# Kernel optimization log

Hardware: AMD Instinct MI355X
Metric: run time of the kernel (lower is better)

Reference implementation:

```python
import jax, jax.numpy as jnp
import numpy as np

# -------- configuration (production-scale segmentation head) --------
BS, C, H, W = 8, 256, 96, 96
N = H * W          # nodes in the spanning tree (flattened pixels)
E = N - 1          # spanning-tree edge count
ZETA_G = 0.01      # default zeta_g of Global_APro.forward


def setup_inputs() -> dict:
    key = jax.random.key(0)
    k1, k2 = jax.random.split(key)
    feature_in = jax.random.normal(k1, (BS, 1, H, W), dtype=jnp.float32)
    # scaled so norm2 distances over C=256 channels stay O(1..10)
    embed_in = 0.1 * jax.random.normal(k2, (BS, C, H, W), dtype=jnp.float32)
    # Random spanning trees, one per batch element. Edges are topologically
    # ordered: edge e connects parent=src[e] < child=tgt[e]=e+1, so processing
    # edges in order is a valid root->leaf sweep (and reversed is leaf->root).
    rng = np.random.default_rng(0)
    trees = []
    children = np.arange(1, N, dtype=np.int32)
    for _ in range(BS):
        parents = np.floor(rng.random(E) * np.arange(1, N)).astype(np.int32)
        trees.append(np.stack([parents, children], axis=1))
    tree = jnp.asarray(np.stack(trees, axis=0))  # [BS, E, 2] int32
    return {"feature_in": feature_in, "embed_in": embed_in, "tree": tree}


def _gp_single(f, wgt, src, tgt):
    """Global affinity propagation (tree filter) on one tree.
    Computes out_i = sum_j A_ij f_j / sum_j A_ij with A_ij = prod of edge
    affinities along the unique tree path i->j, via the classic two-pass DP.
    f: [N], wgt/src/tgt: [E] (edges topologically ordered, parent=src).
    """
    ones = jnp.ones_like(f)

    def up(carry, xs):                 # leaf -> root aggregation
        S, Z = carry
        s, t, we = xs
        S = S.at[s].add(we * S[t])
        Z = Z.at[s].add(we * Z[t])
        return (S, Z), None

    (S, Z), _ = jax.lax.scan(up, (f, ones), (src, tgt, wgt), reverse=True)

    def down(carry, xs):               # root -> leaf propagation
        F, G = carry
        s, t, we = xs
        F = F.at[t].set(we * F[s] + (1.0 - we * we) * F[t])
        G = G.at[t].set(we * G[s] + (1.0 - we * we) * G[t])
        return (F, G), None

    (F, G), _ = jax.lax.scan(down, (S, Z), (src, tgt, wgt))
    return F / G


def reference(feature_in, embed_in, tree):
    bs, c, h, w = embed_in.shape
    n = h * w
    emb = embed_in.reshape(bs, c, n)               # [bs, c, N]
    src = tree[:, :, 0]                            # [bs, E]
    tgt = tree[:, :, 1]                            # [bs, E]
    # gather node embeddings along tree edges (get_true_index)
    gather = jax.vmap(lambda e, i: e[:, i])        # [c, N], [E] -> [c, E]
    src_node = gather(emb, src)                    # [bs, c, E]
    tgt_node = gather(emb, tgt)                    # [bs, c, E]
    diff = src_node - tgt_node
    dist = jnp.sum(diff * diff, axis=1)            # norm2_distance -> [bs, E]
    wgt = jnp.exp(-ZETA_G * dist)                  # edge affinity
    f = feature_in.reshape(bs, n)                  # [bs, N]
    out = jax.vmap(_gp_single)(f, wgt, src, tgt)   # [bs, N]
    return out.reshape(bs, 1, h, w)
```

## Files before the change

### kernel.cpp

```cpp
#include <hip/hip_runtime.h>
#include <hip/hip_bf16.h>
#include <hip/hip_fp16.h>

#define BS 8
#define C  256
#define N  9216
#define E  9215
#define MAXD 128
#define LVL_STRIDE 192
#define TSLABS (N / 64)

__global__ __launch_bounds__(1024) void setup_kernel(const float* __restrict__ emb,
                                                     __half* __restrict__ embT,
                                                     const int* __restrict__ tree,
                                                     int* __restrict__ uparr,
                                                     unsigned char* __restrict__ lenG,
                                                     int* __restrict__ lvlOff) {
    __shared__ int P[N];
    __shared__ unsigned int CC[N];
    __shared__ int cnt[MAXD];
    __shared__ int off[MAXD + 1];
    const int tid = threadIdx.x;

    if (blockIdx.x < BS) {
        const int b = blockIdx.x;
        const int* tb = tree + b * E * 2;

        for (int t = tid; t < N; t += 1024) {
            P[t] = (t == 0) ? 0 : (tb[(t - 1) * 2] | (1 << 16));
            CC[t] = 0u;
        }
        for (int i = tid; i < MAXD; i += 1024) cnt[i] = 0;
        __syncthreads();

        for (int it = 0; it < 6; ++it) {
            int np[9];
            int k = 0;
            for (int t = tid; t < N; t += 1024, ++k) {
                int p = P[t];
                int pa = P[p & 0xffff];
                np[k] = (pa & 0xffff) | ((p >> 16) + (pa >> 16)) << 16;
            }
            __syncthreads();
            k = 0;
            for (int t = tid; t < N; t += 1024, ++k) P[t] = np[k];
            __syncthreads();
        }

        for (int t = 1 + tid; t < N; t += 1024) {
            int d = P[t] >> 16; if (d > MAXD - 1) d = MAXD - 1;
            atomicAdd(&cnt[d], 1);
            int p = tb[(t - 1) * 2];
            atomicAdd(&CC[p], 1u);
        }
        __syncthreads();
        if (tid == 0) {
            int acc = 0, mx = 1;
            for (int d = 0; d < MAXD; ++d) {
                off[d] = acc; acc += cnt[d];
                if (cnt[d] > 0) mx = d;
            }
            off[MAXD] = acc;
            lvlOff[b * LVL_STRIDE + MAXD + 1] = mx;
        }
        __syncthreads();
        for (int i = tid; i < MAXD; i += 1024) cnt[i] = 0;
        __syncthreads();

        for (int p = tid; p < N; p += 1024) {
            unsigned int c = CC[p];
            if (c > 0) {
                int dlev = (P[p] >> 16) + 1; if (dlev > MAXD - 1) dlev = MAXD - 1;
                int base = off[dlev] + atomicAdd(&cnt[dlev], (int)c);
                P[p] = (P[p] & 0xffff0000) | base;
            }
        }
        for (int i = tid; i < N; i += 1024) lenG[b * N + i] = 0;
        __syncthreads();

        for (int p = tid; p < N; p += 1024) {
            unsigned int c = CC[p];
            if (c > 0) {
                int base = P[p] & 0xffff;
                unsigned char fl = (c > 2u) ? 4 : 0;
                for (unsigned int j = 0; j < c; j += 2) {
                    unsigned char ln = (j + 2 <= c) ? 2 : 1;
                    lenG[b * N + base + j] = ln | fl;
                }
            }
        }
        __syncthreads();

        for (int t = 1 + tid; t < N; t += 1024) {
            int p = tb[(t - 1) * 2];
            unsigned int o = atomicSub(&CC[p], 1u) - 1u;
            int slot = (P[p] & 0xffff) + (int)o;
            uparr[b * N + slot] = t | (p << 16);
        }
        for (int i = tid; i <= MAXD; i += 1024) lvlOff[b * LVL_STRIDE + i] = off[i];
    } else {
        const int tb = blockIdx.x - BS;
        const int b  = tb & 7;
        const int n0 = (tb >> 3) * 64;
        __half (*tile)[65] = (__half(*)[65])P;

        const int nn = tid & 63;
        const int cg = tid >> 6;
        const float* src = emb + (size_t)b * C * N + n0;
        #pragma unroll
        for (int k = 0; k < 16; ++k) {
            int cc = cg * 16 + k;
            tile[cc][nn] = __float2half(src[(size_t)cc * N + nn]);
        }
        __syncthreads();

        const int cp = tid & 127;
        const int ng = tid >> 7;
        __half* dst = embT + ((size_t)b * N + n0) * C;
        #pragma unroll
        for (int k = 0; k < 8; ++k) {
            int n2 = ng * 8 + k;
            __half2 v = __halves2half2(tile[2 * cp][n2], tile[2 * cp + 1][n2]);
            *(__half2*)(dst + (size_t)n2 * C + 2 * cp) = v;
        }
    }
}

__global__ __launch_bounds__(256) void weights_kernel(const __half* __restrict__ embT,
                                                      const int* __restrict__ tree,
                                                      float* __restrict__ wgt) {
    const int b   = blockIdx.y;
    const int tid = threadIdx.x;
    const int lane = tid & 63;
    const int wid  = tid >> 6;
    const int sub  = lane >> 5;
    const int l    = lane & 31;
    const int e    = (blockIdx.x * 4 + wid) * 2 + sub;

    float acc = 0.f;
    if (e < E) {
        int s = tree[(b * E + e) * 2];
        int t = tree[(b * E + e) * 2 + 1];
        const float4* ps = (const float4*)(embT + ((size_t)b * N + s) * C) + l;
        const float4* pt = (const float4*)(embT + ((size_t)b * N + t) * C) + l;
        float4 av = *ps;
        float4 bv = *pt;
        const __half2* ah = (const __half2*)&av;
        const __half2* bh = (const __half2*)&bv;
        #pragma unroll
        for (int j = 0; j < 4; ++j) {
            float2 fa = __half22float2(ah[j]);
            float2 fb = __half22float2(bh[j]);
            float d0 = fa.x - fb.x;
            float d1 = fa.y - fb.y;
            acc += d0 * d0 + d1 * d1;
        }
    }
    #pragma unroll
    for (int m = 16; m >= 1; m >>= 1) acc += __shfl_xor(acc, m);
    if (l == 0 && e < E) wgt[b * N + e] = __expf(-0.01f * acc);
}

__global__ __launch_bounds__(1024) void dp_kernel(const float* __restrict__ feat,
                                                  const int* __restrict__ lvlOff,
                                                  const int* __restrict__ uparr,
                                                  const unsigned char* __restrict__ lenG,
                                                  const float* __restrict__ wgt,
                                                  float* __restrict__ out) {
    const int b = blockIdx.x;
    const int tid = threadIdx.x;
    __shared__ float2 V[N];
    __shared__ int2 TSW[N];
    __shared__ unsigned char LEN[N];
    __shared__ int off[MAXD + 1];
    __shared__ int maxd_s;

    for (int i = tid; i <= MAXD; i += 1024) off[i] = lvlOff[b * LVL_STRIDE + i];
    if (tid == 0) maxd_s = lvlOff[b * LVL_STRIDE + MAXD + 1];

    const int* tsA = uparr + b * N;
    const float* wG = wgt + b * N;
    const unsigned char* lG = lenG + b * N;
    for (int i = tid; i < N; i += 1024) {
        V[i] = make_float2(feat[b * N + i], 1.0f);
        LEN[i] = lG[i];
    }
    for (int i = tid; i < E; i += 1024) {
        int ts = tsA[i];
        float w = wG[(ts & 0xffff) - 1];
        TSW[i] = make_int2(ts, __float_as_int(w));
    }
    __syncthreads();
    const int maxd = maxd_s;

    int s1 = off[maxd + 1];
    for (int lev = maxd; lev >= 1; --lev) {
        int s0 = off[lev];
        for (int i = s0 + tid; i < s1; i += 1024) {
            int lb = LEN[i];
            if (lb) {
                int2 e0 = TSW[i];
                int p = e0.x >> 16;
                float w0 = __int_as_float(e0.y);
                float2 v0 = V[e0.x & 0xffff];
                float ax = w0 * v0.x, ay = w0 * v0.y;
                if (lb & 2) {
                    int2 e1 = TSW[i + 1];
                    float w1 = __int_as_float(e1.y);
                    float2 v1 = V[e1.x & 0xffff];
                    ax += w1 * v1.x; ay += w1 * v1.y;
                }
                if (lb & 4) {
                    atomicAdd(&V[p].x, ax);
                    atomicAdd(&V[p].y, ay);
                } else {
                    float2 vp = V[p];
                    V[p] = make_float2(vp.x + ax, vp.y + ay);
                }
            }
        }
        s1 = s0;
        __syncthreads();
    }
    int s0 = off[1];
    for (int lev = 1; lev <= maxd; ++lev) {
        int s1d = off[lev + 1];
        for (int i = s0 + tid; i < s1d; i += 1024) {
            int2 ew = TSW[i];
            int t = ew.x & 0xffff, s = ew.x >> 16;
            float w = __int_as_float(ew.y);
            float2 vs = V[s], vt = V[t];
            float c = 1.f - w * w;
            V[t] = make_float2(w * vs.x + c * vt.x, w * vs.y + c * vt.y);
        }
        s0 = s1d;
        __syncthreads();
    }
    for (int i = tid; i < N; i += 1024) {
        float2 v = V[i];
        out[b * N + i] = v.x / v.y;
    }
}

extern "C" void kernel_launch(void* const* d_in, const int* in_sizes, int n_in,
                              void* d_out, int out_size, void* d_ws, size_t ws_size,
                              hipStream_t stream) {
    const float* feat = (const float*)d_in[0];
    const float* emb  = (const float*)d_in[1];
    const int*   tree = (const int*)d_in[2];
    float* out = (float*)d_out;

    const size_t BN = (size_t)BS * N;
    float* wgt    = (float*)d_ws;
    int*   uparr  = (int*)((char*)d_ws + BN * 4);
    int*   lvlOff = (int*)((char*)d_ws + BN * 8);
    unsigned char* lenG = (unsigned char*)((char*)d_ws + BN * 8 + BS * LVL_STRIDE * 4);
    __half* embT  = (__half*)((char*)d_ws +
                     ((BN * 9 + BS * LVL_STRIDE * 4 + 255) / 256) * 256);

    setup_kernel<<<BS + TSLABS * BS, 1024, 0, stream>>>(emb, embT, tree, uparr, lenG, lvlOff);
    weights_kernel<<<dim3((E + 7) / 8, BS), 256, 0, stream>>>(embT, tree, wgt);
    dp_kernel<<<BS, 1024, 0, stream>>>(feat, lvlOff, uparr, lenG, wgt, out);
}
```

Baseline: 171.4 us.

## Overlap tree-level setup with edge-weight computation and prefetch DP level data

The transpose now runs as its own kernel. Tree depth and level bucketing move into a kernel that also computes the edge weights, so the serial per-tree setup blocks overlap with the weight blocks. Setup replaces the tid==0 serial offset scan with per-subgroup counters and a parallel prefix scan, and uses ping-pong pointer jumping without a register staging array. The DP kernel loads LEN as ints and prefetches the next level's edge records into registers before processing the current level, hiding LDS latency between barriers. Costs are more register pressure and more complex indexing.

```diff
diff --git a/kernel.cpp b/kernel.cpp
--- a/kernel.cpp
+++ b/kernel.cpp
@@ -10,156 +10,203 @@
 #define LVL_STRIDE 192
 #define TSLABS (N / 64)
 
-__global__ __launch_bounds__(1024) void setup_kernel(const float* __restrict__ emb,
-                                                     __half* __restrict__ embT,
-                                                     const int* __restrict__ tree,
-                                                     int* __restrict__ uparr,
-                                                     unsigned char* __restrict__ lenG,
-                                                     int* __restrict__ lvlOff) {
+__global__ __launch_bounds__(1024) void transpose_kernel(const float* __restrict__ emb,
+                                                         __half* __restrict__ embT) {
+    const int tb = blockIdx.x;
+    const int b  = tb & 7;
+    const int n0 = (tb >> 3) * 64;
+    __shared__ __half tile[256][65];
+    const int tid = threadIdx.x;
+
+    const int nn = tid & 63;
+    const int cg = tid >> 6;
+    const float* src = emb + (size_t)b * C * N + n0;
+    #pragma unroll
+    for (int k = 0; k < 16; ++k) {
+        int cc = cg * 16 + k;
+        tile[cc][nn] = __float2half(src[(size_t)cc * N + nn]);
+    }
+    __syncthreads();
+
+    const int cp = tid & 127;
+    const int ng = tid >> 7;
+    __half* dst = embT + ((size_t)b * N + n0) * C;
+    #pragma unroll
+    for (int k = 0; k < 8; ++k) {
+        int n2 = ng * 8 + k;
+        __half2 v = __halves2half2(tile[2 * cp][n2], tile[2 * cp + 1][n2]);
+        *(__half2*)(dst + (size_t)n2 * C + 2 * cp) = v;
+    }
+}
+
+__global__ __launch_bounds__(1024) void wl_kernel(const __half* __restrict__ embT,
+                                                  const int* __restrict__ tree,
+                                                  float* __restrict__ wgt,
+                                                  int* __restrict__ uparr,
+                                                  unsigned char* __restrict__ lenG,
+                                                  int* __restrict__ lvlOff) {
     __shared__ int P[N];
-    __shared__ unsigned int CC[N];
-    __shared__ int cnt[MAXD];
+    __shared__ int Q[N];
+    __shared__ int cnt8[MAXD * 8];
+    __shared__ int tot[MAXD];
+    __shared__ int sc1[MAXD];
     __shared__ int off[MAXD + 1];
+    __shared__ int maxd_sh;
     const int tid = threadIdx.x;
 
-    if (blockIdx.x < BS) {
-        const int b = blockIdx.x;
-        const int* tb = tree + b * E * 2;
-
+    if (blockIdx.x >= BS) {
+        const int wb = blockIdx.x - BS;
+        const int b  = wb & 7;
+        const int l  = tid & 31;
+        const int e  = (wb >> 3) * 32 + (tid >> 5);
+        if (e < E) {
+            int s = tree[(b * E + e) * 2];
+            int t = tree[(b * E + e) * 2 + 1];
+            const float4* ps = (const float4*)(embT + ((size_t)b * N + s) * C) + l;
+            const float4* pt = (const float4*)(embT + ((size_t)b * N + t) * C) + l;
+            float4 av = *ps;
+            float4 bv = *pt;
+            const __half2* ah = (const __half2*)&av;
+            const __half2* bh = (const __half2*)&bv;
+            float acc = 0.f;
+            #pragma unroll
+            for (int j = 0; j < 4; ++j) {
+                float2 fa = __half22float2(ah[j]);
+                float2 fb = __half22float2(bh[j]);
+                float d0 = fa.x - fb.x;
+                float d1 = fa.y - fb.y;
+                acc += d0 * d0 + d1 * d1;
+            }
+            #pragma unroll
+            for (int m = 16; m >= 1; m >>= 1) acc += __shfl_xor(acc, m);
+            if (l == 0) wgt[b * N + e] = __expf(-0.01f * acc);
+        }
+        return;
+    }
+
+    const int b = blockIdx.x;
+    const int* tb = tree + b * E * 2;
+
+    for (int t = tid; t < N; t += 1024)
+        P[t] = (t == 0) ? 0 : (tb[(t - 1) * 2] | (1 << 16));
+    for (int i = tid; i < MAXD * 8; i += 1024) cnt8[i] = 0;
+    {
+        int* lz = (int*)(lenG + b * N);
+        for (int i = tid; i < N / 4; i += 1024) lz[i] = 0;
+    }
+    if (tid == 0) maxd_sh = 1;
+    __syncthreads();
+
+    for (int r = 0; r < 3; ++r) {
         for (int t = tid; t < N; t += 1024) {
-            P[t] = (t == 0) ? 0 : (tb[(t - 1) * 2] | (1 << 16));
-            CC[t] = 0u;
-        }
-        for (int i = tid; i < MAXD; i += 1024) cnt[i] = 0;
+            int p = P[t];
+            int pa = P[p & 0xffff];
+            Q[t] = (pa & 0xffff) | (((p >> 16) + (pa >> 16)) << 16);
+        }
         __syncthreads();
-
-        for (int it = 0; it < 6; ++it) {
-            int np[9];
-            int k = 0;
-            for (int t = tid; t < N; t += 1024, ++k) {
-                int p = P[t];
-                int pa = P[p & 0xffff];
-                np[k] = (pa & 0xffff) | ((p >> 16) + (pa >> 16)) << 16;
-            }
-            __syncthreads();
-            k = 0;
-            for (int t = tid; t < N; t += 1024, ++k) P[t] = np[k];
-            __syncthreads();
-        }
-
-        for (int t = 1 + tid; t < N; t += 1024) {
-            int d = P[t] >> 16; if (d > MAXD - 1) d = MAXD - 1;
-            atomicAdd(&cnt[d], 1);
-            int p = tb[(t - 1) * 2];
-            atomicAdd(&CC[p], 1u);
+        for (int t = tid; t < N; t += 1024) {
+            int p = Q[t];
+            int pa = Q[p & 0xffff];
+            P[t] = (pa & 0xffff) | (((p >> 16) + (pa >> 16)) << 16);
         }
         __syncthreads();
-        if (tid == 0) {
-            int acc = 0, mx = 1;
-            for (int d = 0; d < MAXD; ++d) {
-                off[d] = acc; acc += cnt[d];
-                if (cnt[d] > 0) mx = d;
-            }
-            off[MAXD] = acc;
-            lvlOff[b * LVL_STRIDE + MAXD + 1] = mx;
-        }
-        __syncthreads();
-        for (int i = tid; i < MAXD; i += 1024) cnt[i] = 0;
-        __syncthreads();
-
-        for (int p = tid; p < N; p += 1024) {
-            unsigned int c = CC[p];
-            if (c > 0) {
-                int dlev = (P[p] >> 16) + 1; if (dlev > MAXD - 1) dlev = MAXD - 1;
-                int base = off[dlev] + atomicAdd(&cnt[dlev], (int)c);
-                P[p] = (P[p] & 0xffff0000) | base;
-            }
-        }
-        for (int i = tid; i < N; i += 1024) lenG[b * N + i] = 0;
-        __syncthreads();
-
-        for (int p = tid; p < N; p += 1024) {
-            unsigned int c = CC[p];
-            if (c > 0) {
-                int base = P[p] & 0xffff;
-                unsigned char fl = (c > 2u) ? 4 : 0;
-                for (unsigned int j = 0; j < c; j += 2) {
-                    unsigned char ln = (j + 2 <= c) ? 2 : 1;
-                    lenG[b * N + base + j] = ln | fl;
-                }
-            }
-        }
-        __syncthreads();
-
-        for (int t = 1 + tid; t < N; t += 1024) {
-            int p = tb[(t - 1) * 2];
-            unsigned int o = atomicSub(&CC[p], 1u) - 1u;
-            int slot = (P[p] & 0xffff) + (int)o;
-            uparr[b * N + slot] = t | (p << 16);
-        }
-        for (int i = tid; i <= MAXD; i += 1024) lvlOff[b * LVL_STRIDE + i] = off[i];
-    } else {
-        const int tb = blockIdx.x - BS;
-        const int b  = tb & 7;
-        const int n0 = (tb >> 3) * 64;
-        __half (*tile)[65] = (__half(*)[65])P;
-
-        const int nn = tid & 63;
-        const int cg = tid >> 6;
-        const float* src = emb + (size_t)b * C * N + n0;
-        #pragma unroll
-        for (int k = 0; k < 16; ++k) {
-            int cc = cg * 16 + k;
-            tile[cc][nn] = __float2half(src[(size_t)cc * N + nn]);
-        }
-        __syncthreads();
-
-        const int cp = tid & 127;
-        const int ng = tid >> 7;
-        __half* dst = embT + ((size_t)b * N + n0) * C;
+    }
+
+    for (int t = tid; t < N; t += 1024) Q[t] = 0;
+    __syncthreads();
+    for (int t = 1 + tid; t < N; t += 1024) atomicAdd(&Q[tb[(t - 1) * 2]], 1);
+    __syncthreads();
+
+    for (int p = tid; p < N; p += 1024) {
+        int c = Q[p];
+        int dep = P[p] >> 16;
+        if (c > 0) {
+            int dlev = dep + 1;
+            int sub = tid >> 7;
+            int lo = atomicAdd(&cnt8[dlev * 8 + sub], c);
+            P[p] = (dep << 25) | (sub << 22) | lo;
+        } else {
+            P[p] = (dep << 25);
+        }
+    }
+    __syncthreads();
+
+    for (int d = tid; d < MAXD; d += 1024) {
+        int s = 0;
         #pragma unroll
         for (int k = 0; k < 8; ++k) {
-            int n2 = ng * 8 + k;
-            __half2 v = __halves2half2(tile[2 * cp][n2], tile[2 * cp + 1][n2]);
-            *(__half2*)(dst + (size_t)n2 * C + 2 * cp) = v;
-        }
-    }
+            int v = cnt8[d * 8 + k];
+            cnt8[d * 8 + k] = s;
+            s += v;
+        }
+        tot[d] = s;
+        if (s > 0) atomicMax(&maxd_sh, d);
+    }
+    __syncthreads();
+
+    {
+        int* src = tot; int* dst = sc1;
+        for (int step = 1; step < MAXD; step <<= 1) {
+            for (int d = tid; d < MAXD; d += 1024)
+                dst[d] = src[d] + ((d >= step) ? src[d - step] : 0);
+            __syncthreads();
+            int* tmp = src; src = dst; dst = tmp;
+        }
+        for (int d = tid; d < MAXD; d += 1024) off[d + 1] = src[d];
+        if (tid == 0) off[0] = 0;
+    }
+    __syncthreads();
+
+    for (int p = tid; p < N; p += 1024) {
+        int c = Q[p];
+        if (c > 0) {
+            int v = P[p];
+            int dep = ((unsigned)v) >> 25;
+            int sub = (v >> 22) & 7;
+            int lo  = v & 0x3FFF;
+            int dlev = dep + 1;
+            int base = off[dlev] + cnt8[dlev * 8 + sub] + lo;
+            P[p] = (dep << 25) | base;
+            unsigned char fl = (c > 2) ? 4 : 0;
+            for (int j = 0; j < c; j += 2)
+                lenG[b * N + base + j] = (unsigned char)(((j + 2 <= c) ? 2 : 1) | fl);
+        }
+    }
+    __syncthreads();
+
+    for (int t = 1 + tid; t < N; t += 1024) {
+        int p = tb[(t - 1) * 2];
+        unsigned int o = atomicSub((unsigned int*)&Q[p], 1u) - 1u;
+        int slot = (P[p] & 0x3FFF) + (int)o;
+        uparr[b * N + slot] = t | (p << 16);
+    }
+    for (int i = tid; i <= MAXD; i += 1024) lvlOff[b * LVL_STRIDE + i] = off[i];
+    if (tid == 0) lvlOff[b * LVL_STRIDE + MAXD + 1] = maxd_sh;
 }
 
-__global__ __launch_bounds__(256) void weights_kernel(const __half* __restrict__ embT,
-                                                      const int* __restrict__ tree,
-                                                      float* __restrict__ wgt) {
-    const int b   = blockIdx.y;
-    const int tid = threadIdx.x;
-    const int lane = tid & 63;
-    const int wid  = tid >> 6;
-    const int sub  = lane >> 5;
-    const int l    = lane & 31;
-    const int e    = (blockIdx.x * 4 + wid) * 2 + sub;
-
-    float acc = 0.f;
-    if (e < E) {
-        int s = tree[(b * E + e) * 2];
-        int t = tree[(b * E + e) * 2 + 1];
-        const float4* ps = (const float4*)(embT + ((size_t)b * N + s) * C) + l;
-        const float4* pt = (const float4*)(embT + ((size_t)b * N + t) * C) + l;
-        float4 av = *ps;
-        float4 bv = *pt;
-        const __half2* ah = (const __half2*)&av;
-        const __half2* bh = (const __half2*)&bv;
-        #pragma unroll
-        for (int j = 0; j < 4; ++j) {
-            float2 fa = __half22float2(ah[j]);
-            float2 fb = __half22float2(bh[j]);
-            float d0 = fa.x - fb.x;
-            float d1 = fa.y - fb.y;
-            acc += d0 * d0 + d1 * d1;
-        }
-    }
-    #pragma unroll
-    for (int m = 16; m >= 1; m >>= 1) acc += __shfl_xor(acc, m);
-    if (l == 0 && e < E) wgt[b * N + e] = __expf(-0.01f * acc);
-}
+#define UP_PROCESS(e0, e1, lb)                                                \
+    if (lb) {                                                                 \
+        int p_ = (e0).x >> 16;                                                \
+        float w0_ = __int_as_float((e0).y);                                   \
+        float2 v0_ = V[(e0).x & 0xffff];                                      \
+        float ax_ = w0_ * v0_.x, ay_ = w0_ * v0_.y;                           \
+        if ((lb) & 2) {                                                       \
+            float w1_ = __int_as_float((e1).y);                               \
+            float2 v1_ = V[(e1).x & 0xffff];                                  \
+            ax_ += w1_ * v1_.x; ay_ += w1_ * v1_.y;                           \
+        }                                                                     \
+        if ((lb) & 4) { atomicAdd(&V[p_].x, ax_); atomicAdd(&V[p_].y, ay_); } \
+        else { float2 vp_ = V[p_]; V[p_] = make_float2(vp_.x + ax_, vp_.y + ay_); } \
+    }
+
+#define DOWN_PROCESS(g)                                                       \
+    {                                                                         \
+        int t_ = (g).x & 0xffff, s_ = (g).x >> 16;                            \
+        float w_ = __int_as_float((g).y);                                     \
+        float2 vs_ = V[s_], vt_ = V[t_];                                      \
+        float c_ = 1.f - w_ * w_;                                             \
+        V[t_] = make_float2(w_ * vs_.x + c_ * vt_.x, w_ * vs_.y + c_ * vt_.y); \
+    }
 
 __global__ __launch_bounds__(1024) void dp_kernel(const float* __restrict__ feat,
                                                   const int* __restrict__ lvlOff,
@@ -171,7 +218,7 @@
     const int tid = threadIdx.x;
     __shared__ float2 V[N];
     __shared__ int2 TSW[N];
-    __shared__ unsigned char LEN[N];
+    __shared__ __align__(16) unsigned char LEN[N];
     __shared__ int off[MAXD + 1];
     __shared__ int maxd_s;
 
@@ -180,11 +227,11 @@
 
     const int* tsA = uparr + b * N;
     const float* wG = wgt + b * N;
-    const unsigned char* lG = lenG + b * N;
-    for (int i = tid; i < N; i += 1024) {
+    const int* lG4 = (const int*)(lenG + b * N);
+    for (int i = tid; i < N; i += 1024)
         V[i] = make_float2(feat[b * N + i], 1.0f);
-        LEN[i] = lG[i];
-    }
+    for (int i = tid; i < N / 4; i += 1024)
+        ((int*)LEN)[i] = lG4[i];
     for (int i = tid; i < E; i += 1024) {
         int ts = tsA[i];
         float w = wG[(ts & 0xffff) - 1];
@@ -194,48 +241,70 @@
     const int maxd = maxd_s;
 
     int s1 = off[maxd + 1];
+    int s0 = off[maxd];
+    int pns0 = (maxd >= 2) ? off[maxd - 1] : 0;
+    int2 eA0, eA1, eB0, eB1; int lbA, lbB;
+    {
+        int i0 = s0 + tid, i1 = i0 + 1024;
+        int c0 = (i0 < s1) ? i0 : 0;
+        int c1 = (i1 < s1) ? i1 : 0;
+        lbA = (i0 < s1) ? LEN[c0] : 0;
+        lbB = (i1 < s1) ? LEN[c1] : 0;
+        eA0 = TSW[c0]; eA1 = TSW[c0 + 1];
+        eB0 = TSW[c1]; eB1 = TSW[c1 + 1];
+    }
     for (int lev = maxd; lev >= 1; --lev) {
-        int s0 = off[lev];
-        for (int i = s0 + tid; i < s1; i += 1024) {
+        int ns0 = pns0, ns1 = s0;
+        pns0 = (lev >= 2) ? off[lev - 2] : 0;
+        int2 fA0, fA1, fB0, fB1; int nlbA = 0, nlbB = 0;
+        fA0 = fA1 = fB0 = fB1 = make_int2(0, 0);
+        if (lev > 1) {
+            int i0 = ns0 + tid, i1 = i0 + 1024;
+            int c0 = (i0 < ns1) ? i0 : 0;
+            int c1 = (i1 < ns1) ? i1 : 0;
+            nlbA = (i0 < ns1) ? LEN[c0] : 0;
+            nlbB = (i1 < ns1) ? LEN[c1] : 0;
+            fA0 = TSW[c0]; fA1 = TSW[c0 + 1];
+            fB0 = TSW[c1]; fB1 = TSW[c1 + 1];
+        }
+        UP_PROCESS(eA0, eA1, lbA);
+        UP_PROCESS(eB0, eB1, lbB);
+        for (int i = s0 + tid + 2048; i < s1; i += 1024) {
             int lb = LEN[i];
-            if (lb) {
-                int2 e0 = TSW[i];
-                int p = e0.x >> 16;
-                float w0 = __int_as_float(e0.y);
-                float2 v0 = V[e0.x & 0xffff];
-                float ax = w0 * v0.x, ay = w0 * v0.y;
-                if (lb & 2) {
-                    int2 e1 = TSW[i + 1];
-                    float w1 = __int_as_float(e1.y);
-                    float2 v1 = V[e1.x & 0xffff];
-                    ax += w1 * v1.x; ay += w1 * v1.y;
-                }
-                if (lb & 4) {
-                    atomicAdd(&V[p].x, ax);
-                    atomicAdd(&V[p].y, ay);
-                } else {
-                    float2 vp = V[p];
-                    V[p] = make_float2(vp.x + ax, vp.y + ay);
-                }
-            }
-        }
-        s1 = s0;
+            int2 g0 = TSW[i]; int2 g1 = TSW[i + 1];
+            UP_PROCESS(g0, g1, lb);
+        }
         __syncthreads();
-    }
-    int s0 = off[1];
+        s0 = ns0; s1 = ns1;
+        eA0 = fA0; eA1 = fA1; eB0 = fB0; eB1 = fB1; lbA = nlbA; lbB = nlbB;
+    }
+
+    int d0 = off[1], d1 = off[2];
+    bool vA, vB; int2 gA, gB;
+    {
+        int i0 = d0 + tid, i1 = i0 + 1024;
+        vA = i0 < d1; vB = i1 < d1;
+        gA = TSW[vA ? i0 : 0]; gB = TSW[vB ? i1 : 0];
+    }
     for (int lev = 1; lev <= maxd; ++lev) {
-        int s1d = off[lev + 1];
-        for (int i = s0 + tid; i < s1d; i += 1024) {
-            int2 ew = TSW[i];
-            int t = ew.x & 0xffff, s = ew.x >> 16;
-            float w = __int_as_float(ew.y);
-            float2 vs = V[s], vt = V[t];
-            float c = 1.f - w * w;
-            V[t] = make_float2(w * vs.x + c * vt.x, w * vs.y + c * vt.y);
-        }
-        s0 = s1d;
+        int nd0 = d1;
+        int nd1 = off[(lev + 2 <= MAXD) ? lev + 2 : MAXD];
+        bool nvA = false, nvB = false; int2 hA = gA, hB = gB;
+        if (lev < maxd) {
+            int i0 = nd0 + tid, i1 = i0 + 1024;
+            nvA = i0 < nd1; nvB = i1 < nd1;
+            hA = TSW[nvA ? i0 : 0]; hB = TSW[nvB ? i1 : 0];
+        }
+        if (vA) DOWN_PROCESS(gA);
+        if (vB) DOWN_PROCESS(gB);
+        for (int i = d0 + tid + 2048; i < d1; i += 1024) {
+            int2 g = TSW[i];
+            DOWN_PROCESS(g);
+        }
         __syncthreads();
-    }
+        d0 = nd0; d1 = nd1; vA = nvA; vB = nvB; gA = hA; gB = hB;
+    }
+
     for (int i = tid; i < N; i += 1024) {
         float2 v = V[i];
         out[b * N + i] = v.x / v.y;
@@ -258,7 +327,7 @@
     __half* embT  = (__half*)((char*)d_ws +
                      ((BN * 9 + BS * LVL_STRIDE * 4 + 255) / 256) * 256);
 
-    setup_kernel<<<BS + TSLABS * BS, 1024, 0, stream>>>(emb, embT, tree, uparr, lenG, lvlOff);
-    weights_kernel<<<dim3((E + 7) / 8, BS), 256, 0, stream>>>(embT, tree, wgt);
+    transpose_kernel<<<TSLABS * BS, 1024, 0, stream>>>(emb, embT);
+    wl_kernel<<<BS + ((E + 31) / 32) * BS, 1024, 0, stream>>>(embT, tree, wgt, uparr, lenG, lvlOff);
     dp_kernel<<<BS, 1024, 0, stream>>>(feat, lvlOff, uparr, lenG, wgt, out);
 }
```

Result: slower. 180.0 us (+5.0%).

## Run narrow tree levels on a single wavefront and parallelize level offset setup

Applied to the files above, without the earlier changes.

The DP kernel now finds the shallow and deep levels that hold at most 64 slots and handles them with a single 64-lane wavefront. Those levels use a block-local fence instead of a full block barrier, cutting the many __syncthreads in the level-by-level sweeps. The DP block shrinks to 512 threads. Setup replaces the serial per-thread-0 level scan with per-subgroup counters and a parallel prefix scan, merges the child counts into a ping-pong buffer, and zeroes the length array with word stores. The single-wave sections depend on lockstep wavefront execution for ordering between levels.

```diff
diff --git a/kernel.cpp b/kernel.cpp
--- a/kernel.cpp
+++ b/kernel.cpp
@@ -9,6 +9,7 @@
 #define MAXD 128
 #define LVL_STRIDE 192
 #define TSLABS (N / 64)
+#define NARROW 64
 
 __global__ __launch_bounds__(1024) void setup_kernel(const float* __restrict__ emb,
                                                      __half* __restrict__ embT,
@@ -17,88 +18,15 @@
                                                      unsigned char* __restrict__ lenG,
                                                      int* __restrict__ lvlOff) {
     __shared__ int P[N];
-    __shared__ unsigned int CC[N];
-    __shared__ int cnt[MAXD];
+    __shared__ int Q[N];
+    __shared__ int cnt8[MAXD * 8];
+    __shared__ int tot[MAXD];
+    __shared__ int sc1[MAXD];
     __shared__ int off[MAXD + 1];
+    __shared__ int maxd_sh;
     const int tid = threadIdx.x;
 
-    if (blockIdx.x < BS) {
-        const int b = blockIdx.x;
-        const int* tb = tree + b * E * 2;
-
-        for (int t = tid; t < N; t += 1024) {
-            P[t] = (t == 0) ? 0 : (tb[(t - 1) * 2] | (1 << 16));
-            CC[t] = 0u;
-        }
-        for (int i = tid; i < MAXD; i += 1024) cnt[i] = 0;
-        __syncthreads();
-
-        for (int it = 0; it < 6; ++it) {
-            int np[9];
-            int k = 0;
-            for (int t = tid; t < N; t += 1024, ++k) {
-                int p = P[t];
-                int pa = P[p & 0xffff];
-                np[k] = (pa & 0xffff) | ((p >> 16) + (pa >> 16)) << 16;
-            }
-            __syncthreads();
-            k = 0;
-            for (int t = tid; t < N; t += 1024, ++k) P[t] = np[k];
-            __syncthreads();
-        }
-
-        for (int t = 1 + tid; t < N; t += 1024) {
-            int d = P[t] >> 16; if (d > MAXD - 1) d = MAXD - 1;
-            atomicAdd(&cnt[d], 1);
-            int p = tb[(t - 1) * 2];
-            atomicAdd(&CC[p], 1u);
-        }
-        __syncthreads();
-        if (tid == 0) {
-            int acc = 0, mx = 1;
-            for (int d = 0; d < MAXD; ++d) {
-                off[d] = acc; acc += cnt[d];
-                if (cnt[d] > 0) mx = d;
-            }
-            off[MAXD] = acc;
-            lvlOff[b * LVL_STRIDE + MAXD + 1] = mx;
-        }
-        __syncthreads();
-        for (int i = tid; i < MAXD; i += 1024) cnt[i] = 0;
-        __syncthreads();
-
-        for (int p = tid; p < N; p += 1024) {
-            unsigned int c = CC[p];
-            if (c > 0) {
-                int dlev = (P[p] >> 16) + 1; if (dlev > MAXD - 1) dlev = MAXD - 1;
-                int base = off[dlev] + atomicAdd(&cnt[dlev], (int)c);
-                P[p] = (P[p] & 0xffff0000) | base;
-            }
-        }
-        for (int i = tid; i < N; i += 1024) lenG[b * N + i] = 0;
-        __syncthreads();
-
-        for (int p = tid; p < N; p += 1024) {
-            unsigned int c = CC[p];
-            if (c > 0) {
-                int base = P[p] & 0xffff;
-                unsigned char fl = (c > 2u) ? 4 : 0;
-                for (unsigned int j = 0; j < c; j += 2) {
-                    unsigned char ln = (j + 2 <= c) ? 2 : 1;
-                    lenG[b * N + base + j] = ln | fl;
-                }
-            }
-        }
-        __syncthreads();
-
-        for (int t = 1 + tid; t < N; t += 1024) {
-            int p = tb[(t - 1) * 2];
-            unsigned int o = atomicSub(&CC[p], 1u) - 1u;
-            int slot = (P[p] & 0xffff) + (int)o;
-            uparr[b * N + slot] = t | (p << 16);
-        }
-        for (int i = tid; i <= MAXD; i += 1024) lvlOff[b * LVL_STRIDE + i] = off[i];
-    } else {
+    if (blockIdx.x >= BS) {
         const int tb = blockIdx.x - BS;
         const int b  = tb & 7;
         const int n0 = (tb >> 3) * 64;
@@ -123,7 +51,116 @@
             __half2 v = __halves2half2(tile[2 * cp][n2], tile[2 * cp + 1][n2]);
             *(__half2*)(dst + (size_t)n2 * C + 2 * cp) = v;
         }
-    }
+        return;
+    }
+
+    const int b = blockIdx.x;
+    const int* tb = tree + b * E * 2;
+
+    for (int t = tid; t < N; t += 1024)
+        P[t] = (t == 0) ? 0 : (tb[(t - 1) * 2] | (1 << 16));
+    for (int i = tid; i < MAXD * 8; i += 1024) cnt8[i] = 0;
+    {
+        int* lz = (int*)(lenG + b * N);
+        for (int i = tid; i < N / 4; i += 1024) lz[i] = 0;
+    }
+    if (tid == 0) maxd_sh = 1;
+    __syncthreads();
+
+    for (int r = 0; r < 3; ++r) {
+        for (int t = tid; t < N; t += 1024) {
+            int p = P[t];
+            int pa = P[p & 0xffff];
+            Q[t] = (pa & 0xffff) | (((p >> 16) + (pa >> 16)) << 16);
+        }
+        __syncthreads();
+        for (int t = tid; t < N; t += 1024) {
+            int p = Q[t];
+            int pa = Q[p & 0xffff];
+            P[t] = (pa & 0xffff) | (((p >> 16) + (pa >> 16)) << 16);
+        }
+        __syncthreads();
+    }
+
+    for (int t = tid; t < N; t += 1024) Q[t] = 0;
+    __syncthreads();
+    for (int t = 1 + tid; t < N; t += 1024) atomicAdd(&Q[tb[(t - 1) * 2]], 1);
+    __syncthreads();
+
+    for (int p = tid; p < N; p += 1024) {
+        int c = Q[p];
+        int dep = P[p] >> 16;
+        if (c > 0) {
+            int dlev = dep + 1;
+            int sub = tid >> 7;
+            int lo = atomicAdd(&cnt8[dlev * 8 + sub], c);
+            P[p] = (dep << 25) | (sub << 22) | lo;
+        } else {
+            P[p] = (dep << 25);
+        }
+    }
+    __syncthreads();
+
+    for (int d = tid; d < MAXD; d += 1024) {
+        int s = 0;
+        #pragma unroll
+        for (int k = 0; k < 8; ++k) {
+            int v = cnt8[d * 8 + k];
+            cnt8[d * 8 + k] = s;
+            s += v;
+        }
+        tot[d] = s;
+        if (s > 0) atomicMax(&maxd_sh, d);
+    }
+    __syncthreads();
+
+    {
+        int* src = tot; int* dst = sc1;
+        for (int step = 1; step < MAXD; step <<= 1) {
+            for (int d = tid; d < MAXD; d += 1024)
+                dst[d] = src[d] + ((d >= step) ? src[d - step] : 0);
+            __syncthreads();
+            int* tmp = src; src = dst; dst = tmp;
+        }
+        for (int d = tid; d < MAXD; d += 1024) off[d + 1] = src[d];
+        if (tid == 0) off[0] = 0;
+    }
+    __syncthreads();
+
+    if (tid == 0) {
+        int md = maxd_sh;
+        int lo = 0;
+        while (lo < md && off[lo + 2] - off[lo + 1] <= NARROW) ++lo;
+        int hi = md + 1;
+        while (hi > lo + 1 && off[hi] - off[hi - 1] <= NARROW) --hi;
+        lvlOff[b * LVL_STRIDE + 129] = md;
+        lvlOff[b * LVL_STRIDE + 130] = lo;
+        lvlOff[b * LVL_STRIDE + 131] = hi;
+    }
+    for (int p = tid; p < N; p += 1024) {
+        int c = Q[p];
+        if (c > 0) {
+            int v = P[p];
+            int dep = ((unsigned)v) >> 25;
+            int sub = (v >> 22) & 7;
+            int lo  = v & 0x3FFF;
+            int dlev = dep + 1;
+            int base = off[dlev] + cnt8[dlev * 8 + sub] + lo;
+            P[p] = (dep << 25) | base;
+            unsigned char fl = (c > 2) ? 4 : 0;
+            for (int j = 0; j < c; j += 2)
+                lenG[b * N + base + j] = (unsigned char)(((j + 2 <= c) ? 2 : 1) | fl);
+        }
+    }
+    __syncthreads();
+
+    for (int t = 1 + tid; t < N; t += 1024) {
+        int p = tb[(t - 1) * 2];
+        unsigned int o = atomicSub((unsigned int*)&Q[p], 1u) - 1u;
+        int slot = (P[p] & 0x3FFF) + (int)o;
+        uparr[b * N + slot] = t | (p << 16);
+    }
+    for (int i = tid; i <= MAXD; i += 1024) lvlOff[b * LVL_STRIDE + i] = off[i];
 }
 
 __global__ __launch_bounds__(256) void weights_kernel(const __half* __restrict__ embT,
@@ -161,82 +198,118 @@
     if (l == 0 && e < E) wgt[b * N + e] = __expf(-0.01f * acc);
 }
 
-__global__ __launch_bounds__(1024) void dp_kernel(const float* __restrict__ feat,
-                                                  const int* __restrict__ lvlOff,
-                                                  const int* __restrict__ uparr,
-                                                  const unsigned char* __restrict__ lenG,
-                                                  const float* __restrict__ wgt,
-                                                  float* __restrict__ out) {
+__device__ __forceinline__ void up_slot(float2* V, const int2* TSW,
+                                        const unsigned char* LEN, int i) {
+    int lb = LEN[i];
+    if (lb) {
+        int2 e0 = TSW[i];
+        int p = e0.x >> 16;
+        float w0 = __int_as_float(e0.y);
+        float2 v0 = V[e0.x & 0xffff];
+        float ax = w0 * v0.x, ay = w0 * v0.y;
+        if (lb & 2) {
+            int2 e1 = TSW[i + 1];
+            float w1 = __int_as_float(e1.y);
+            float2 v1 = V[e1.x & 0xffff];
+            ax += w1 * v1.x; ay += w1 * v1.y;
+        }
+        if (lb & 4) {
+            atomicAdd(&V[p].x, ax);
+            atomicAdd(&V[p].y, ay);
+        } else {
+            float2 vp = V[p];
+            V[p] = make_float2(vp.x + ax, vp.y + ay);
+        }
+    }
+}
+
+__device__ __forceinline__ void down_slot(float2* V, const int2* TSW, int i) {
+    int2 g = TSW[i];
+    int t = g.x & 0xffff, s = g.x >> 16;
+    float w = __int_as_float(g.y);
+    float2 vs = V[s], vt = V[t];
+    float c = 1.f - w * w;
+    V[t] = make_float2(w * vs.x + c * vt.x, w * vs.y + c * vt.y);
+}
+
+__global__ __launch_bounds__(512) void dp_kernel(const float* __restrict__ feat,
+                                                 const int* __restrict__ lvlOff,
+                                                 const int* __restrict__ uparr,
+                                                 const unsigned char* __restrict__ lenG,
+                                                 const float* __restrict__ wgt,
+                                                 float* __restrict__ out) {
     const int b = blockIdx.x;
     const int tid = threadIdx.x;
     __shared__ float2 V[N];
     __shared__ int2 TSW[N];
-    __shared__ unsigned char LEN[N];
+    __shared__ __align__(16) unsigned char LEN[N];
     __shared__ int off[MAXD + 1];
-    __shared__ int maxd_s;
-
-    for (int i = tid; i <= MAXD; i += 1024) off[i] = lvlOff[b * LVL_STRIDE + i];
-    if (tid == 0) maxd_s = lvlOff[b * LVL_STRIDE + MAXD + 1];
+    __shared__ int meta[3];
+
+    for (int i = tid; i <= MAXD; i += 512) off[i] = lvlOff[b * LVL_STRIDE + i];
+    if (tid < 3) meta[tid] = lvlOff[b * LVL_STRIDE + 129 + tid];
 
     const int* tsA = uparr + b * N;
     const float* wG = wgt + b * N;
-    const unsigned char* lG = lenG + b * N;
-    for (int i = tid; i < N; i += 1024) {
+    for (int i = tid; i < N; i += 512)
         V[i] = make_float2(feat[b * N + i], 1.0f);
-        LEN[i] = lG[i];
-    }
-    for (int i = tid; i < E; i += 1024) {
+    {
+        const int* lG4 = (const int*)(lenG + b * N);
+        for (int i = tid; i < N / 4; i += 512) ((int*)LEN)[i] = lG4[i];
+    }
+    for (int i = tid; i < E; i += 512) {
         int ts = tsA[i];
         float w = wG[(ts & 0xffff) - 1];
         TSW[i] = make_int2(ts, __float_as_int(w));
     }
     __syncthreads();
-    const int maxd = maxd_s;
-
-    int s1 = off[maxd + 1];
-    for (int lev = maxd; lev >= 1; --lev) {
-        int s0 = off[lev];
-        for (int i = s0 + tid; i < s1; i += 1024) {
-            int lb = LEN[i];
-            if (lb) {
-                int2 e0 = TSW[i];
-                int p = e0.x >> 16;
-                float w0 = __int_as_float(e0.y);
-                float2 v0 = V[e0.x & 0xffff];
-                float ax = w0 * v0.x, ay = w0 * v0.y;
-                if (lb & 2) {
-                    int2 e1 = TSW[i + 1];
-                    float w1 = __int_as_float(e1.y);
-                    float2 v1 = V[e1.x & 0xffff];
-                    ax += w1 * v1.x; ay += w1 * v1.y;
-                }
-                if (lb & 4) {
-                    atomicAdd(&V[p].x, ax);
-                    atomicAdd(&V[p].y, ay);
-                } else {
-                    float2 vp = V[p];
-                    V[p] = make_float2(vp.x + ax, vp.y + ay);
-                }
-            }
-        }
-        s1 = s0;
-        __syncthreads();
-    }
-    int s0 = off[1];
-    for (int lev = 1; lev <= maxd; ++lev) {
-        int s1d = off[lev + 1];
-        for (int i = s0 + tid; i < s1d; i += 1024) {
-            int2 ew = TSW[i];
-            int t = ew.x & 0xffff, s = ew.x >> 16;
-            float w = __int_as_float(ew.y);
-            float2 vs = V[s], vt = V[t];
-            float c = 1.f - w * w;
-            V[t] = make_float2(w * vs.x + c * vt.x, w * vs.y + c * vt.y);
-        }
-        s0 = s1d;
-        __syncthreads();
-    }
-    for (int i = tid; i < N; i += 1024) {
+    const int maxd = meta[0], loE = meta[1], hiS = meta[2];
+
+    if (tid < 64) {
+        for (int lev = maxd; lev >= hiS; --lev) {
+            int s0 = off[lev], s1 = off[lev + 1];
+            for (int i = s0 + tid; i < s1; i += 64) up_slot(V, TSW, LEN, i);
+            __threadfence_block();
+        }
+    }
+    __syncthreads();
+    for (int lev = hiS - 1; lev > loE; --lev) {
+        int s0 = off[lev], s1 = off[lev + 1];
+        for (int i = s0 + tid; i < s1; i += 512) up_slot(V, TSW, LEN, i);
+        __syncthreads();
+    }
+    if (tid < 64) {
+        for (int lev = loE; lev >= 1; --lev) {
+            int s0 = off[lev], s1 = off[lev + 1];
+            for (int i = s0 + tid; i < s1; i += 64) up_slot(V, TSW, LEN, i);
+            __threadfence_block();
+        }
+    }
+    __syncthreads();
+
+    if (tid < 64) {
+        for (int lev = 1; lev <= loE; ++lev) {
+            int s0 = off[lev], s1 = off[lev + 1];
+            for (int i = s0 + tid; i < s1; i += 64) down_slot(V, TSW, i);
+            __threadfence_block();
+        }
+    }
+    __syncthreads();
+    for (int lev = loE + 1; lev < hiS; ++lev) {
+        int s0 = off[lev], s1 = off[lev + 1];
+        for (int i = s0 + tid; i < s1; i += 512) down_slot(V, TSW, i);
+        __syncthreads();
+    }
+    if (tid < 64) {
+        for (int lev = hiS; lev <= maxd; ++lev) {
+            int s0 = off[lev], s1 = off[lev + 1];
+            for (int i = s0 + tid; i < s1; i += 64) down_slot(V, TSW, i);
+            __threadfence_block();
+        }
+    }
+    __syncthreads();
+
+    for (int i = tid; i < N; i += 512) {
         float2 v = V[i];
         out[b * N + i] = v.x / v.y;
     }
@@ -260,5 +333,5 @@
 
     setup_kernel<<<BS + TSLABS * BS, 1024, 0, stream>>>(emb, embT, tree, uparr, lenG, lvlOff);
     weights_kernel<<<dim3((E + 7) / 8, BS), 256, 0, stream>>>(embT, tree, wgt);
-    dp_kernel<<<BS, 1024, 0, stream>>>(feat, lvlOff, uparr, lenG, wgt, out);
-}
+    dp_kernel<<<BS, 512, 0, stream>>>(feat, lvlOff, uparr, lenG, wgt, out);
+}
```

After: 171.2 us. About the same (-0.1%).
